# Kernel tuning notes

Hardware: AMD Instinct MI355X
Metric: run time of the kernel (lower is better)

## Reference

```python
import jax, jax.numpy as jnp
import numpy as np

U, I, D, L, NNZ, B = 100000, 50000, 64, 3, 3200000, 4096
N = U + I
MOMENTUM = 0.05

def setup_inputs() -> dict:
    key = jax.random.key(0)
    ks = jax.random.split(key, 10)
    return {
        'user_emb': jax.random.normal(ks[0], (U, D), jnp.float32) * 0.02,
        'item_emb': jax.random.normal(ks[1], (I, D), jnp.float32) * 0.02,
        'W': jax.random.normal(ks[2], (D, D), jnp.float32) * (1.0 / np.sqrt(D)),
        'b': jnp.zeros((D,), jnp.float32),
        'adj_rows': jax.random.randint(ks[3], (NNZ,), 0, N, jnp.int32),
        'adj_cols': jax.random.randint(ks[4], (NNZ,), 0, N, jnp.int32),
        'adj_vals': jax.random.uniform(ks[5], (NNZ,), jnp.float32) * 0.05,
        'users': jax.random.randint(ks[6], (B,), 0, U, jnp.int32),
        'items': jax.random.randint(ks[7], (B,), 0, I, jnp.int32),
        'u_his': jax.random.normal(ks[8], (U, D), jnp.float32),
        'i_his': jax.random.normal(ks[9], (I, D), jnp.float32),
    }

def _spmm(rows, cols, vals, x):
    # y = A @ x for sparse COO A: gather source rows, scale, scatter-add to dest rows
    return jax.ops.segment_sum(vals[:, None] * x[cols], rows, num_segments=N)

def reference(user_emb, item_emb, W, b, adj_rows, adj_cols, adj_vals, users, items, u_his, i_his):
    ego = jnp.concatenate([user_emb, item_emb], axis=0)  # [N, D]
    acc = ego
    cur = ego
    for _ in range(L):
        cur = _spmm(adj_rows, adj_cols, adj_vals, cur)
        acc = acc + cur
    all_emb = acc / (L + 1)           # mean over stacked layers
    u_all = all_emb[:U]
    i_all = all_emb[U:]
    u_online = u_all[users]           # [B, D]
    i_online = i_all[items]
    m = MOMENTUM
    u_target = jax.lax.stop_gradient(u_his[users] * m + u_online * (1.0 - m))
    i_target = jax.lax.stop_gradient(i_his[items] * m + i_online * (1.0 - m))
    p_u = u_online @ W.T + b
    p_i = i_online @ W.T + b
    return (p_u, u_target, p_i, i_target)
```

## Files before the change

### kernel.cpp

```cpp
#include <hip/hip_runtime.h>
#include <hip/hip_bf16.h>

#define U_CNT   100000
#define I_CNT   50000
#define D_DIM   64
#define N_NODES 150000
#define NNZ_E   3200000
#define B_SZ    4096

#define SUPER_SHIFT 12
#define NSUP 37
#define TILE1_E 4096
#define N_TILES1 ((NNZ_E + TILE1_E - 1) / TILE1_E)
#define TILE2_E 2048

#define CAP_SUP 98304
#define CAP2 4096
#define NSUB (NSUP * 32)
#define P2_BLOCKS_PER_SUP 24

typedef unsigned int uint;
typedef unsigned short ushort_t;
typedef _Float16 half_t;
typedef half_t half2_t __attribute__((ext_vector_type(2)));

union h2u_t { uint u; half2_t h; };
__device__ __forceinline__ half2_t u2h2(uint u) { h2u_t c; c.u = u; return c.h; }
__device__ __forceinline__ uint h22u(half2_t h) { h2u_t c; c.h = h; return c.u; }
__device__ __forceinline__ half2_t h2shfl_xor(half2_t v, int m) {
    h2u_t c; c.h = v; c.u = (uint)__shfl_xor((int)c.u, m, 64); return c.h;
}
__device__ __forceinline__ float h2lo(uint u) { return (float)u2h2(u)[0]; }
__device__ __forceinline__ float h2hi(uint u) { return (float)u2h2(u)[1]; }

__global__ __launch_bounds__(256) void convert_kernel(const float4* __restrict__ ue4,
                                                      const float4* __restrict__ ie4,
                                                      uint2* __restrict__ e2) {
    int g = blockIdx.x * 256 + threadIdx.x;
    if (g >= N_NODES * 16) return;
    float4 f = (g < U_CNT * 16) ? ue4[g] : ie4[g - U_CNT * 16];
    half2_t a = { (half_t)f.x, (half_t)f.y };
    half2_t b = { (half_t)f.z, (half_t)f.w };
    uint2 o; o.x = h22u(a); o.y = h22u(b);
    e2[g] = o;
}

__global__ __launch_bounds__(256) void init_cursors_kernel(int* __restrict__ scursor,
                                                           int* __restrict__ subcursor) {
    int i = blockIdx.x * 256 + threadIdx.x;
    if (i < NSUP) scursor[i] = i * CAP_SUP;
    if (i < NSUB) subcursor[i] = i * CAP2;
}

__global__ __launch_bounds__(256) void super_scatter_kernel(const int* __restrict__ rows,
                                                            const int* __restrict__ cols,
                                                            const float* __restrict__ vals,
                                                            int* __restrict__ scursor,
                                                            int2* __restrict__ smeta) {
    __shared__ int2 stage[TILE1_E];
    __shared__ int lcnt[NSUP];
    __shared__ int lbase[NSUP];
    __shared__ int gbase[NSUP];
    int tid = threadIdx.x;

    for (int tile = blockIdx.x; tile < N_TILES1; tile += gridDim.x) {
        int base = tile * TILE1_E;
        int cnt_tile = NNZ_E - base;
        if (cnt_tile > TILE1_E) cnt_tile = TILE1_E;

        if (tid < NSUP) lcnt[tid] = 0;
        __syncthreads();

        int nk = cnt_tile - tid;
        nk = (nk <= 0) ? 0 : (nk + 255) >> 8;

        int pk[16]; float vv[16]; int sp[16]; int rk[16];
        #pragma unroll
        for (int k = 0; k < 16; ++k) {
            if (k < nk) {
                int j = base + tid + (k << 8);
                int r = rows[j];
                int c = cols[j];
                vv[k] = vals[j];
                sp[k] = r >> SUPER_SHIFT;
                pk[k] = ((r & ((1 << SUPER_SHIFT) - 1)) << 18) | c;
                rk[k] = atomicAdd(&lcnt[sp[k]], 1);
            }
        }
        __syncthreads();

        if (tid < 64) {
            int c = (tid < NSUP) ? lcnt[tid] : 0;
            int incl = c;
            #pragma unroll
            for (int off = 1; off < 64; off <<= 1) {
                int t = __shfl_up(incl, off, 64);
                if (tid >= off) incl += t;
            }
            if (tid < NSUP) {
                lbase[tid] = incl - c;
                gbase[tid] = atomicAdd(&scursor[tid], c);
            }
        }
        __syncthreads();

        #pragma unroll
        for (int k = 0; k < 16; ++k) {
            if (k < nk) stage[lbase[sp[k]] + rk[k]] = make_int2(pk[k], __float_as_int(vv[k]));
        }
        __syncthreads();

        int wv = tid >> 6, ln = tid & 63;
        for (int s = wv; s < NSUP; s += 4) {
            int c = lcnt[s], lb = lbase[s], gb = gbase[s];
            int lim = (s + 1) * CAP_SUP;
            for (int t = ln; t < c; t += 64)
                if (gb + t < lim) smeta[gb + t] = stage[lb + t];
        }
        __syncthreads();
    }
}

__global__ __launch_bounds__(256) void sub_scatter_kernel(const int2* __restrict__ smeta,
                                                          const int* __restrict__ scursor,
                                                          int* __restrict__ subcursor,
                                                          int2* __restrict__ meta) {
    __shared__ int2 stage[TILE2_E];
    __shared__ int lcnt[32];
    __shared__ int lbase[32];
    __shared__ int gbase[32];
    int tid = threadIdx.x;
    int s    = blockIdx.x / P2_BLOCKS_PER_SUP;
    int slot = blockIdx.x % P2_BLOCKS_PER_SUP;
    int beg = s * CAP_SUP;
    int cnt_s = scursor[s] - beg;
    if (cnt_s > CAP_SUP) cnt_s = CAP_SUP;
    int end = beg + cnt_s;

    for (int tb = beg + slot * TILE2_E; tb < end; tb += P2_BLOCKS_PER_SUP * TILE2_E) {
        int cnt_tile = end - tb;
        if (cnt_tile > TILE2_E) cnt_tile = TILE2_E;

        if (tid < 32) lcnt[tid] = 0;
        __syncthreads();

        int nk = cnt_tile - tid;
        nk = (nk <= 0) ? 0 : (nk + 255) >> 8;

        int2 ed[8]; int sb[8]; int rk[8];
        #pragma unroll
        for (int k = 0; k < 8; ++k) {
            if (k < nk) {
                ed[k] = smeta[tb + tid + (k << 8)];
                sb[k] = ((uint)ed[k].x >> 25) & 31;
                rk[k] = atomicAdd(&lcnt[sb[k]], 1);
            }
        }
        __syncthreads();

        if (tid < 64) {
            int c = (tid < 32) ? lcnt[tid] : 0;
            int incl = c;
            #pragma unroll
            for (int off = 1; off < 32; off <<= 1) {
                int t = __shfl_up(incl, off, 64);
                if (tid >= off) incl += t;
            }
            if (tid < 32) {
                lbase[tid] = incl - c;
                gbase[tid] = atomicAdd(&subcursor[(s << 5) + tid], c);
            }
        }
        __syncthreads();

        #pragma unroll
        for (int k = 0; k < 8; ++k) {
            if (k < nk) stage[lbase[sb[k]] + rk[k]] = ed[k];
        }
        __syncthreads();

        int wv = tid >> 6, ln = tid & 63;
        for (int b = wv; b < 32; b += 4) {
            int c = lcnt[b], lb = lbase[b], gb = gbase[b];
            int lim = ((s << 5) + b + 1) * CAP2;
            for (int t = ln; t < c; t += 64)
                if (gb + t < lim) meta[gb + t] = stage[lb + t];
        }
        __syncthreads();
    }
}

__global__ __launch_bounds__(256) void row_sort_kernel(const int* __restrict__ subcursor,
                                                       int2* __restrict__ meta,
                                                       int* __restrict__ rstart,
                                                       int* __restrict__ rend) {
    __shared__ int2 stage[CAP2];
    __shared__ int rcnt[128];
    __shared__ int scan[128];
    __shared__ int cur[128];
    int g = blockIdx.x;
    int base = g * CAP2;
    int cnt = subcursor[g] - base;
    if (cnt > CAP2) cnt = CAP2;
    int tid = threadIdx.x;
    int s = g >> 5, q = g & 31;
    int r0 = (s << SUPER_SHIFT) + (q << 7);

    if (tid < 128) rcnt[tid] = 0;
    __syncthreads();

    for (int i = tid; i < cnt; i += 256) {
        int2 e = meta[base + i];
        stage[i] = e;
        atomicAdd(&rcnt[((uint)e.x >> 18) & 127], 1);
    }
    __syncthreads();

    if (tid < 128) scan[tid] = rcnt[tid];
    __syncthreads();
    for (int off = 1; off < 128; off <<= 1) {
        int t = (tid < 128 && tid >= off) ? scan[tid - off] : 0;
        __syncthreads();
        if (tid < 128) scan[tid] += t;
        __syncthreads();
    }
    if (tid < 128) {
        int excl = scan[tid] - rcnt[tid];
        cur[tid] = excl;
        int r = r0 + tid;
        if (r < N_NODES) {
            rstart[r] = base + excl;
            rend[r]   = base + scan[tid];
        }
    }
    __syncthreads();

    for (int i = tid; i < cnt; i += 256) {
        int2 e = stage[i];
        int rl = ((uint)e.x >> 18) & 127;
        int pos = atomicAdd(&cur[rl], 1);
        float v = __int_as_float(e.y);
        half2_t hv = { (half_t)v, (half_t)v };
        meta[base + pos] = make_int2(e.x & 0x3FFFF, (int)h22u(hv));
    }
}

__global__ __launch_bounds__(256) void spmm_fp16_kernel(const int* __restrict__ rstart,
                                                        const int* __restrict__ rend,
                                                        const int2* __restrict__ csr,
                                                        const ushort_t* __restrict__ x,
                                                        ushort_t* __restrict__ out) {
    int wid  = (blockIdx.x * blockDim.x + threadIdx.x) >> 6;
    int lane = threadIdx.x & 63;
    int sub  = lane >> 3;
    int l8   = lane & 7;
    if (wid >= N_NODES) return;
    int s = rstart[wid], e = rend[wid];

    half2_t a0 = { (half_t)0, (half_t)0 };
    half2_t a1 = a0, a2 = a0, a3 = a0;

    int j = s + sub;
    int2 cv = (j < e) ? csr[j] : make_int2(0, 0);
    for (; j < e; j += 8) {
        int jn = j + 8;
        int2 nx = (jn < e) ? csr[jn] : make_int2(0, 0);
        half2_t vv = u2h2((uint)cv.y);
        uint4 xv = ((const uint4*)x)[(size_t)cv.x * 8 + l8];
        a0 += u2h2(xv.x) * vv;
        a1 += u2h2(xv.y) * vv;
        a2 += u2h2(xv.z) * vv;
        a3 += u2h2(xv.w) * vv;
        cv = nx;
    }
    a0 += h2shfl_xor(a0, 8);  a1 += h2shfl_xor(a1, 8);
    a2 += h2shfl_xor(a2, 8);  a3 += h2shfl_xor(a3, 8);
    a0 += h2shfl_xor(a0, 16); a1 += h2shfl_xor(a1, 16);
    a2 += h2shfl_xor(a2, 16); a3 += h2shfl_xor(a3, 16);
    a0 += h2shfl_xor(a0, 32); a1 += h2shfl_xor(a1, 32);
    a2 += h2shfl_xor(a2, 32); a3 += h2shfl_xor(a3, 32);

    if (sub == 0) {
        uint4 r;
        r.x = h22u(a0); r.y = h22u(a1); r.z = h22u(a2); r.w = h22u(a3);
        ((uint4*)out)[(size_t)wid * 8 + l8] = r;
    }
}

__global__ __launch_bounds__(256) void epilogue_kernel(const int* __restrict__ users,
                                                       const int* __restrict__ items,
                                                       const int* __restrict__ rstart,
                                                       const int* __restrict__ rend,
                                                       const int2* __restrict__ csr,
                                                       const ushort_t* __restrict__ ebuf,
                                                       const ushort_t* __restrict__ buf1,
                                                       const ushort_t* __restrict__ buf2,
                                                       const float* __restrict__ u_his,
                                                       const float* __restrict__ i_his,
                                                       const float* __restrict__ W,
                                                       const float* __restrict__ bvec,
                                                       float* __restrict__ out) {
    __shared__ float Wt[D_DIM * 65];
    __shared__ float bsh[D_DIM];
    __shared__ float on_s[4][D_DIM];
    for (int t = threadIdx.x; t < D_DIM * D_DIM; t += blockDim.x) {
        int j = t >> 6, k = t & 63;
        Wt[k * 65 + j] = W[t];
    }
    if (threadIdx.x < D_DIM) bsh[threadIdx.x] = bvec[threadIdx.x];

    int wv   = threadIdx.x >> 6;
    int wid  = blockIdx.x * 4 + wv;
    int lane = threadIdx.x & 63;
    int sub  = lane >> 4;
    int l16  = lane & 15;

    bool is_user = (wid < B_SZ);
    int  samp = is_user ? wid : wid - B_SZ;
    int  idx  = is_user ? users[samp] : items[samp];
    int  row  = is_user ? idx : (U_CNT + idx);

    int s = rstart[row], e = rend[row];
    half2_t c0 = { (half_t)0, (half_t)0 };
    half2_t c1 = c0;
    for (int j = s + sub; j < e; j += 4) {
        int2 cv = csr[j];
        half2_t vv = u2h2((uint)cv.y);
        uint2 xv = ((const uint2*)buf2)[(size_t)cv.x * 16 + l16];
        c0 += u2h2(xv.x) * vv;
        c1 += u2h2(xv.y) * vv;
    }
    c0 += h2shfl_xor(c0, 16); c1 += h2shfl_xor(c1, 16);
    c0 += h2shfl_xor(c0, 32); c1 += h2shfl_xor(c1, 32);

    if (sub == 0) {
        uint2 eg = ((const uint2*)ebuf)[(size_t)row * 16 + l16];
        uint2 b1 = ((const uint2*)buf1)[(size_t)row * 16 + l16];
        uint2 b2 = ((const uint2*)buf2)[(size_t)row * 16 + l16];
        on_s[wv][l16 * 4 + 0] = (h2lo(eg.x) + h2lo(b1.x) + h2lo(b2.x) + (float)c0[0]) * 0.25f;
        on_s[wv][l16 * 4 + 1] = (h2hi(eg.x) + h2hi(b1.x) + h2hi(b2.x) + (float)c0[1]) * 0.25f;
        on_s[wv][l16 * 4 + 2] = (h2lo(eg.y) + h2lo(b1.y) + h2lo(b2.y) + (float)c1[0]) * 0.25f;
        on_s[wv][l16 * 4 + 3] = (h2hi(eg.y) + h2hi(b1.y) + h2hi(b2.y) + (float)c1[1]) * 0.25f;
    }
    __syncthreads();

    float online = on_s[wv][lane];
    const float* his = is_user ? u_his : i_his;
    float target = 0.05f * his[(size_t)idx * D_DIM + lane] + 0.95f * online;

    float p = bsh[lane];
    #pragma unroll
    for (int k = 0; k < D_DIM; ++k) {
        float ok = __shfl(online, k, 64);
        p = fmaf(ok, Wt[k * 65 + lane], p);
    }

    size_t base = is_user ? 0 : (size_t)2 * B_SZ * D_DIM;
    out[base + (size_t)samp * D_DIM + lane] = p;
    out[base + (size_t)B_SZ * D_DIM + (size_t)samp * D_DIM + lane] = target;
}


extern "C" void kernel_launch(void* const* d_in, const int* in_sizes, int n_in,
                              void* d_out, int out_size, void* d_ws, size_t ws_size,
                              hipStream_t stream) {
    const float* user_emb = (const float*)d_in[0];
    const float* item_emb = (const float*)d_in[1];
    const float* W        = (const float*)d_in[2];
    const float* bvec     = (const float*)d_in[3];
    const int*   adj_rows = (const int*)d_in[4];
    const int*   adj_cols = (const int*)d_in[5];
    const float* adj_vals = (const float*)d_in[6];
    const int*   users    = (const int*)d_in[7];
    const int*   items    = (const int*)d_in[8];
    const float* u_his    = (const float*)d_in[9];
    const float* i_his    = (const float*)d_in[10];
    float* out = (float*)d_out;

    char* ws = (char*)d_ws;
    size_t o = 0;
    ushort_t* ebuf  = (ushort_t*)(ws + o); o += (size_t)N_NODES * D_DIM * 2;
    ushort_t* buf1  = (ushort_t*)(ws + o); o += (size_t)N_NODES * D_DIM * 2;
    int2*  smeta    = (int2*)(ws + o);     o += (size_t)NSUP * CAP_SUP * 8;
    int2*  meta     = (int2*)(ws + o);     o += (size_t)NSUB * CAP2 * 8;
    int*   rstart   = (int*)(ws + o);      o += (size_t)N_NODES * 4;
    int*   rend     = (int*)(ws + o);      o += (size_t)N_NODES * 4;
    int*   scursor  = (int*)(ws + o);      o += 64 * 4;
    int*   subcursor= (int*)(ws + o);      o += (size_t)NSUB * 4;
    ushort_t* buf2  = (ushort_t*)smeta;
    (void)ws_size; (void)o; (void)in_sizes; (void)n_in; (void)out_size;

    convert_kernel<<<(N_NODES * 16 + 255) / 256, 256, 0, stream>>>(
        (const float4*)user_emb, (const float4*)item_emb, (uint2*)ebuf);

    init_cursors_kernel<<<(NSUB + 255) / 256, 256, 0, stream>>>(scursor, subcursor);
    super_scatter_kernel<<<N_TILES1, 256, 0, stream>>>(adj_rows, adj_cols, adj_vals,
                                                       scursor, smeta);
    sub_scatter_kernel<<<NSUP * P2_BLOCKS_PER_SUP, 256, 0, stream>>>(smeta, scursor,
                                                                     subcursor, meta);
    row_sort_kernel<<<NSUB, 256, 0, stream>>>(subcursor, meta, rstart, rend);

    int spmm_blocks = (N_NODES + 3) / 4;
    spmm_fp16_kernel<<<spmm_blocks, 256, 0, stream>>>(rstart, rend, meta, ebuf, buf1);
    spmm_fp16_kernel<<<spmm_blocks, 256, 0, stream>>>(rstart, rend, meta, buf1, buf2);

    epilogue_kernel<<<(2 * B_SZ) / 4, 256, 0, stream>>>(users, items, rstart, rend, meta,
                                                        ebuf, buf1, buf2,
                                                        u_his, i_his, W, bvec, out);
}
```

Measured before the change: 349.7 us.

## Fold embedding conversion into scatter kernel and unroll SpMM gather loops

Merges the fp32-to-fp16 embedding conversion into the super-scatter launch as extra blocks, removing one kernel launch and letting the conversion overlap with the COO partitioning. The SpMM and epilogue gather loops are unrolled by four with batched index prefetch, so more independent row loads are in flight per lane. The epilogue also issues its history and self-embedding loads before the neighbour loop. The cost is higher register pressure in the SpMM kernel, which may lower occupancy.

```diff
diff --git a/kernel.cpp b/kernel.cpp
--- a/kernel.cpp
+++ b/kernel.cpp
@@ -19,6 +19,9 @@
 #define NSUB (NSUP * 32)
 #define P2_BLOCKS_PER_SUP 24
 
+#define CONV_THREADS (N_NODES * 16)
+#define CONV_BLOCKS ((CONV_THREADS + 255) / 256)
+
 typedef unsigned int uint;
 typedef unsigned short ushort_t;
 typedef _Float16 half_t;
@@ -33,18 +36,6 @@
 __device__ __forceinline__ float h2lo(uint u) { return (float)u2h2(u)[0]; }
 __device__ __forceinline__ float h2hi(uint u) { return (float)u2h2(u)[1]; }
 
-__global__ __launch_bounds__(256) void convert_kernel(const float4* __restrict__ ue4,
-                                                      const float4* __restrict__ ie4,
-                                                      uint2* __restrict__ e2) {
-    int g = blockIdx.x * 256 + threadIdx.x;
-    if (g >= N_NODES * 16) return;
-    float4 f = (g < U_CNT * 16) ? ue4[g] : ie4[g - U_CNT * 16];
-    half2_t a = { (half_t)f.x, (half_t)f.y };
-    half2_t b = { (half_t)f.z, (half_t)f.w };
-    uint2 o; o.x = h22u(a); o.y = h22u(b);
-    e2[g] = o;
-}
-
 __global__ __launch_bounds__(256) void init_cursors_kernel(int* __restrict__ scursor,
                                                            int* __restrict__ subcursor) {
     int i = blockIdx.x * 256 + threadIdx.x;
@@ -56,68 +47,81 @@
                                                             const int* __restrict__ cols,
                                                             const float* __restrict__ vals,
                                                             int* __restrict__ scursor,
-                                                            int2* __restrict__ smeta) {
+                                                            int2* __restrict__ smeta,
+                                                            const float4* __restrict__ ue4,
+                                                            const float4* __restrict__ ie4,
+                                                            uint2* __restrict__ e2) {
     __shared__ int2 stage[TILE1_E];
     __shared__ int lcnt[NSUP];
     __shared__ int lbase[NSUP];
     __shared__ int gbase[NSUP];
     int tid = threadIdx.x;
 
-    for (int tile = blockIdx.x; tile < N_TILES1; tile += gridDim.x) {
-        int base = tile * TILE1_E;
-        int cnt_tile = NNZ_E - base;
-        if (cnt_tile > TILE1_E) cnt_tile = TILE1_E;
-
-        if (tid < NSUP) lcnt[tid] = 0;
-        __syncthreads();
-
-        int nk = cnt_tile - tid;
-        nk = (nk <= 0) ? 0 : (nk + 255) >> 8;
-
-        int pk[16]; float vv[16]; int sp[16]; int rk[16];
+    if (blockIdx.x >= N_TILES1) {
+        int g = (blockIdx.x - N_TILES1) * 256 + tid;
+        if (g < CONV_THREADS) {
+            float4 f = (g < U_CNT * 16) ? ue4[g] : ie4[g - U_CNT * 16];
+            half2_t a = { (half_t)f.x, (half_t)f.y };
+            half2_t b = { (half_t)f.z, (half_t)f.w };
+            uint2 o; o.x = h22u(a); o.y = h22u(b);
+            e2[g] = o;
+        }
+        return;
+    }
+
+    int tile = blockIdx.x;
+    int base = tile * TILE1_E;
+    int cnt_tile = NNZ_E - base;
+    if (cnt_tile > TILE1_E) cnt_tile = TILE1_E;
+
+    if (tid < NSUP) lcnt[tid] = 0;
+    __syncthreads();
+
+    int nk = cnt_tile - tid;
+    nk = (nk <= 0) ? 0 : (nk + 255) >> 8;
+
+    int pk[16]; float vv[16]; int sp[16]; int rk[16];
+    #pragma unroll
+    for (int k = 0; k < 16; ++k) {
+        if (k < nk) {
+            int j = base + tid + (k << 8);
+            int r = rows[j];
+            int c = cols[j];
+            vv[k] = vals[j];
+            sp[k] = r >> SUPER_SHIFT;
+            pk[k] = ((r & ((1 << SUPER_SHIFT) - 1)) << 18) | c;
+            rk[k] = atomicAdd(&lcnt[sp[k]], 1);
+        }
+    }
+    __syncthreads();
+
+    if (tid < 64) {
+        int c = (tid < NSUP) ? lcnt[tid] : 0;
+        int incl = c;
         #pragma unroll
-        for (int k = 0; k < 16; ++k) {
-            if (k < nk) {
-                int j = base + tid + (k << 8);
-                int r = rows[j];
-                int c = cols[j];
-                vv[k] = vals[j];
-                sp[k] = r >> SUPER_SHIFT;
-                pk[k] = ((r & ((1 << SUPER_SHIFT) - 1)) << 18) | c;
-                rk[k] = atomicAdd(&lcnt[sp[k]], 1);
-            }
-        }
-        __syncthreads();
-
-        if (tid < 64) {
-            int c = (tid < NSUP) ? lcnt[tid] : 0;
-            int incl = c;
-            #pragma unroll
-            for (int off = 1; off < 64; off <<= 1) {
-                int t = __shfl_up(incl, off, 64);
-                if (tid >= off) incl += t;
-            }
-            if (tid < NSUP) {
-                lbase[tid] = incl - c;
-                gbase[tid] = atomicAdd(&scursor[tid], c);
-            }
-        }
-        __syncthreads();
-
-        #pragma unroll
-        for (int k = 0; k < 16; ++k) {
-            if (k < nk) stage[lbase[sp[k]] + rk[k]] = make_int2(pk[k], __float_as_int(vv[k]));
-        }
-        __syncthreads();
-
-        int wv = tid >> 6, ln = tid & 63;
-        for (int s = wv; s < NSUP; s += 4) {
-            int c = lcnt[s], lb = lbase[s], gb = gbase[s];
-            int lim = (s + 1) * CAP_SUP;
-            for (int t = ln; t < c; t += 64)
-                if (gb + t < lim) smeta[gb + t] = stage[lb + t];
-        }
-        __syncthreads();
+        for (int off = 1; off < 64; off <<= 1) {
+            int t = __shfl_up(incl, off, 64);
+            if (tid >= off) incl += t;
+        }
+        if (tid < NSUP) {
+            lbase[tid] = incl - c;
+            gbase[tid] = atomicAdd(&scursor[tid], c);
+        }
+    }
+    __syncthreads();
+
+    #pragma unroll
+    for (int k = 0; k < 16; ++k) {
+        if (k < nk) stage[lbase[sp[k]] + rk[k]] = make_int2(pk[k], __float_as_int(vv[k]));
+    }
+    __syncthreads();
+
+    int wv = tid >> 6, ln = tid & 63;
+    for (int s = wv; s < NSUP; s += 4) {
+        int c = lcnt[s], lb = lbase[s], gb = gbase[s];
+        int lim = (s + 1) * CAP_SUP;
+        for (int t = ln; t < c; t += 64)
+            if (gb + t < lim) smeta[gb + t] = stage[lb + t];
     }
 }
 
@@ -256,22 +260,40 @@
     int l8   = lane & 7;
     if (wid >= N_NODES) return;
     int s = rstart[wid], e = rend[wid];
+    const uint4* x4 = (const uint4*)x;
 
     half2_t a0 = { (half_t)0, (half_t)0 };
     half2_t a1 = a0, a2 = a0, a3 = a0;
 
+    const int2 z = make_int2(0, 0);
     int j = s + sub;
-    int2 cv = (j < e) ? csr[j] : make_int2(0, 0);
-    for (; j < e; j += 8) {
-        int jn = j + 8;
-        int2 nx = (jn < e) ? csr[jn] : make_int2(0, 0);
-        half2_t vv = u2h2((uint)cv.y);
-        uint4 xv = ((const uint4*)x)[(size_t)cv.x * 8 + l8];
-        a0 += u2h2(xv.x) * vv;
-        a1 += u2h2(xv.y) * vv;
-        a2 += u2h2(xv.z) * vv;
-        a3 += u2h2(xv.w) * vv;
-        cv = nx;
+    int2 c0 = (j      < e) ? csr[j]      : z;
+    int2 c1 = (j + 8  < e) ? csr[j + 8]  : z;
+    int2 c2 = (j + 16 < e) ? csr[j + 16] : z;
+    int2 c3 = (j + 24 < e) ? csr[j + 24] : z;
+    for (; j < e; j += 32) {
+        uint4 x0 = x4[(size_t)c0.x * 8 + l8];
+        uint4 x1 = x4[(size_t)c1.x * 8 + l8];
+        uint4 x2 = x4[(size_t)c2.x * 8 + l8];
+        uint4 x3 = x4[(size_t)c3.x * 8 + l8];
+        int jn = j + 32;
+        int2 n0 = (jn      < e) ? csr[jn]      : z;
+        int2 n1 = (jn + 8  < e) ? csr[jn + 8]  : z;
+        int2 n2 = (jn + 16 < e) ? csr[jn + 16] : z;
+        int2 n3 = (jn + 24 < e) ? csr[jn + 24] : z;
+        half2_t v0 = u2h2((uint)c0.y);
+        a0 += u2h2(x0.x) * v0; a1 += u2h2(x0.y) * v0;
+        a2 += u2h2(x0.z) * v0; a3 += u2h2(x0.w) * v0;
+        half2_t v1 = u2h2((uint)c1.y);
+        a0 += u2h2(x1.x) * v1; a1 += u2h2(x1.y) * v1;
+        a2 += u2h2(x1.z) * v1; a3 += u2h2(x1.w) * v1;
+        half2_t v2 = u2h2((uint)c2.y);
+        a0 += u2h2(x2.x) * v2; a1 += u2h2(x2.y) * v2;
+        a2 += u2h2(x2.z) * v2; a3 += u2h2(x2.w) * v2;
+        half2_t v3 = u2h2((uint)c3.y);
+        a0 += u2h2(x3.x) * v3; a1 += u2h2(x3.y) * v3;
+        a2 += u2h2(x3.z) * v3; a3 += u2h2(x3.w) * v3;
+        c0 = n0; c1 = n1; c2 = n2; c3 = n3;
     }
     a0 += h2shfl_xor(a0, 8);  a1 += h2shfl_xor(a1, 8);
     a2 += h2shfl_xor(a2, 8);  a3 += h2shfl_xor(a3, 8);
@@ -320,33 +342,57 @@
     int  idx  = is_user ? users[samp] : items[samp];
     int  row  = is_user ? idx : (U_CNT + idx);
 
+    const float* his = is_user ? u_his : i_his;
+    float hisv = his[(size_t)idx * D_DIM + lane];
+    uint2 eg = make_uint2(0, 0), b1v = eg, b2v = eg;
+    if (sub == 0) {
+        eg  = ((const uint2*)ebuf)[(size_t)row * 16 + l16];
+        b1v = ((const uint2*)buf1)[(size_t)row * 16 + l16];
+        b2v = ((const uint2*)buf2)[(size_t)row * 16 + l16];
+    }
+
     int s = rstart[row], e = rend[row];
     half2_t c0 = { (half_t)0, (half_t)0 };
     half2_t c1 = c0;
-    for (int j = s + sub; j < e; j += 4) {
-        int2 cv = csr[j];
-        half2_t vv = u2h2((uint)cv.y);
-        uint2 xv = ((const uint2*)buf2)[(size_t)cv.x * 16 + l16];
-        c0 += u2h2(xv.x) * vv;
-        c1 += u2h2(xv.y) * vv;
+    const int2 z = make_int2(0, 0);
+    int j = s + sub;
+    int2 e0 = (j      < e) ? csr[j]      : z;
+    int2 e1 = (j + 4  < e) ? csr[j + 4]  : z;
+    int2 e2 = (j + 8  < e) ? csr[j + 8]  : z;
+    int2 e3 = (j + 12 < e) ? csr[j + 12] : z;
+    for (; j < e; j += 16) {
+        uint2 x0 = ((const uint2*)buf2)[(size_t)e0.x * 16 + l16];
+        uint2 x1 = ((const uint2*)buf2)[(size_t)e1.x * 16 + l16];
+        uint2 x2 = ((const uint2*)buf2)[(size_t)e2.x * 16 + l16];
+        uint2 x3 = ((const uint2*)buf2)[(size_t)e3.x * 16 + l16];
+        int jn = j + 16;
+        int2 n0 = (jn      < e) ? csr[jn]      : z;
+        int2 n1 = (jn + 4  < e) ? csr[jn + 4]  : z;
+        int2 n2 = (jn + 8  < e) ? csr[jn + 8]  : z;
+        int2 n3 = (jn + 12 < e) ? csr[jn + 12] : z;
+        half2_t v0 = u2h2((uint)e0.y);
+        c0 += u2h2(x0.x) * v0; c1 += u2h2(x0.y) * v0;
+        half2_t v1 = u2h2((uint)e1.y);
+        c0 += u2h2(x1.x) * v1; c1 += u2h2(x1.y) * v1;
+        half2_t v2 = u2h2((uint)e2.y);
+        c0 += u2h2(x2.x) * v2; c1 += u2h2(x2.y) * v2;
+        half2_t v3 = u2h2((uint)e3.y);
+        c0 += u2h2(x3.x) * v3; c1 += u2h2(x3.y) * v3;
+        e0 = n0; e1 = n1; e2 = n2; e3 = n3;
     }
     c0 += h2shfl_xor(c0, 16); c1 += h2shfl_xor(c1, 16);
     c0 += h2shfl_xor(c0, 32); c1 += h2shfl_xor(c1, 32);
 
     if (sub == 0) {
-        uint2 eg = ((const uint2*)ebuf)[(size_t)row * 16 + l16];
-        uint2 b1 = ((const uint2*)buf1)[(size_t)row * 16 + l16];
-        uint2 b2 = ((const uint2*)buf2)[(size_t)row * 16 + l16];
-        on_s[wv][l16 * 4 + 0] = (h2lo(eg.x) + h2lo(b1.x) + h2lo(b2.x) + (float)c0[0]) * 0.25f;
-        on_s[wv][l16 * 4 + 1] = (h2hi(eg.x) + h2hi(b1.x) + h2hi(b2.x) + (float)c0[1]) * 0.25f;
-        on_s[wv][l16 * 4 + 2] = (h2lo(eg.y) + h2lo(b1.y) + h2lo(b2.y) + (float)c1[0]) * 0.25f;
-        on_s[wv][l16 * 4 + 3] = (h2hi(eg.y) + h2hi(b1.y) + h2hi(b2.y) + (float)c1[1]) * 0.25f;
+        on_s[wv][l16 * 4 + 0] = (h2lo(eg.x) + h2lo(b1v.x) + h2lo(b2v.x) + (float)c0[0]) * 0.25f;
+        on_s[wv][l16 * 4 + 1] = (h2hi(eg.x) + h2hi(b1v.x) + h2hi(b2v.x) + (float)c0[1]) * 0.25f;
+        on_s[wv][l16 * 4 + 2] = (h2lo(eg.y) + h2lo(b1v.y) + h2lo(b2v.y) + (float)c1[0]) * 0.25f;
+        on_s[wv][l16 * 4 + 3] = (h2hi(eg.y) + h2hi(b1v.y) + h2hi(b2v.y) + (float)c1[1]) * 0.25f;
     }
     __syncthreads();
 
     float online = on_s[wv][lane];
-    const float* his = is_user ? u_his : i_his;
-    float target = 0.05f * his[(size_t)idx * D_DIM + lane] + 0.95f * online;
+    float target = 0.05f * hisv + 0.95f * online;
 
     float p = bsh[lane];
     #pragma unroll
@@ -390,12 +436,10 @@
     ushort_t* buf2  = (ushort_t*)smeta;
     (void)ws_size; (void)o; (void)in_sizes; (void)n_in; (void)out_size;
 
-    convert_kernel<<<(N_NODES * 16 + 255) / 256, 256, 0, stream>>>(
+    init_cursors_kernel<<<(NSUB + 255) / 256, 256, 0, stream>>>(scursor, subcursor);
+    super_scatter_kernel<<<N_TILES1 + CONV_BLOCKS, 256, 0, stream>>>(
+        adj_rows, adj_cols, adj_vals, scursor, smeta,
         (const float4*)user_emb, (const float4*)item_emb, (uint2*)ebuf);
-
-    init_cursors_kernel<<<(NSUB + 255) / 256, 256, 0, stream>>>(scursor, subcursor);
-    super_scatter_kernel<<<N_TILES1, 256, 0, stream>>>(adj_rows, adj_cols, adj_vals,
-                                                       scursor, smeta);
     sub_scatter_kernel<<<NSUP * P2_BLOCKS_PER_SUP, 256, 0, stream>>>(smeta, scursor,
                                                                      subcursor, meta);
     row_sort_kernel<<<NSUB, 256, 0, stream>>>(subcursor, meta, rstart, rend);
```

New measurement: 349.6 us. No clear change (-0.0%).
